# Kernel optimization log

Measured on AMD Instinct MI355X. Metric: run time of the kernel, lower is better.

## Reference

```python
import jax, jax.numpy as jnp
import numpy as np

N, E = 50000, 800000
IN_CH, N_HID, OUT_CH = 128, 256, 128
DROPOUT_P = 0.5


def gcn_conv(x, src, dst, ew, W, b, num_nodes):
    # PyG GCNConv with edge_weight: symmetric normalization with self-loops.
    loop = jnp.arange(num_nodes)
    s = jnp.concatenate([src, loop])
    d = jnp.concatenate([dst, loop])
    w = jnp.concatenate([ew, jnp.ones((num_nodes,), ew.dtype)])
    deg = jax.ops.segment_sum(w, d, num_segments=num_nodes)  # [N]
    dinv = jnp.where(deg > 0, jax.lax.rsqrt(deg), 0.0)
    norm = dinv[s] * w * dinv[d]                             # [E+N]
    h = x @ W                                                # [N, out]
    msg = h[s] * norm[:, None]                               # [E+N, out]
    out = jax.ops.segment_sum(msg, d, num_segments=num_nodes)
    return out + b


def setup_inputs() -> dict:
    key = jax.random.key(0)
    ks = jax.random.split(key, 8)
    x = jax.random.normal(ks[0], (N, IN_CH), dtype=jnp.float32)
    edge_index = jax.random.randint(ks[1], (2, E), 0, N, dtype=jnp.int64)
    weight = jax.random.uniform(ks[2], (E,), dtype=jnp.float32)
    # GCNConv params (glorot weights, zero bias)
    s1 = (6.0 / (IN_CH + N_HID)) ** 0.5
    s2 = (6.0 / (N_HID + OUT_CH)) ** 0.5
    W1 = jax.random.uniform(ks[3], (IN_CH, N_HID), jnp.float32, -s1, s1)
    b1 = jnp.zeros((N_HID,), jnp.float32)
    W2 = jax.random.uniform(ks[4], (N_HID, OUT_CH), jnp.float32, -s2, s2)
    b2 = jnp.zeros((OUT_CH,), jnp.float32)
    return {"x": x, "edge_index": edge_index, "weight": weight,
            "W1": W1, "b1": b1, "W2": W2, "b2": b2}


def reference(x, edge_index, weight, W1, b1, W2, b2):
    src, dst = edge_index[0], edge_index[1]
    h = jax.nn.relu(gcn_conv(x, src, dst, weight, W1, b1, N))
    # F.dropout(x, p) with training=True (torch default); fixed key for determinism
    keep = jax.random.bernoulli(jax.random.key(42), 1.0 - DROPOUT_P, h.shape)
    h = jnp.where(keep, h / (1.0 - DROPOUT_P), 0.0)
    return gcn_conv(h, src, dst, weight, W2, b2, N)
```

## Files before the change

### kernel.cpp

```cpp
#include <hip/hip_runtime.h>
#include <hip/hip_bf16.h>
#include <cstdint>

#define INCH 128
#define NHID 256
#define OUTCH 128

typedef unsigned short u16;
typedef unsigned long long u64;
typedef __attribute__((ext_vector_type(8))) short s8v;
typedef __attribute__((ext_vector_type(4))) float f4v;

__device__ __forceinline__ void bsplit(float a, u16& hi, u16& lo) {
    unsigned u = __float_as_uint(a);
    unsigned r = (u + 0x7fffu + ((u >> 16) & 1u)) >> 16;
    hi = (u16)r;
    float res = a - __uint_as_float(r << 16);
    unsigned u2 = __float_as_uint(res);
    lo = (u16)((u2 + 0x7fffu + ((u2 >> 16) & 1u)) >> 16);
}

__device__ __forceinline__ unsigned rotl32(unsigned x, int d) {
    return (x << d) | (x >> (32 - d));
}

__device__ __forceinline__ void threefry2x32(unsigned k0, unsigned k1,
                                             unsigned x0, unsigned x1,
                                             unsigned& o0, unsigned& o1) {
    unsigned ks2 = k0 ^ k1 ^ 0x1BD11BDAu;
#define TF_R(r) { x0 += x1; x1 = rotl32(x1, (r)); x1 ^= x0; }
    x0 += k0; x1 += k1;
    TF_R(13) TF_R(15) TF_R(26) TF_R(6)
    x0 += k1; x1 += ks2 + 1u;
    TF_R(17) TF_R(29) TF_R(16) TF_R(24)
    x0 += ks2; x1 += k0 + 2u;
    TF_R(13) TF_R(15) TF_R(26) TF_R(6)
    x0 += k0; x1 += k1 + 3u;
    TF_R(17) TF_R(29) TF_R(16) TF_R(24)
    x0 += k1; x1 += ks2 + 4u;
    TF_R(13) TF_R(15) TF_R(26) TF_R(6)
    x0 += ks2; x1 += k0 + 5u;
#undef TF_R
    o0 = x0; o1 = x1;
}

__global__ __launch_bounds__(256) void k_mask(unsigned* __restrict__ mask, int nwords) {
    int i = blockIdx.x * 256 + threadIdx.x;
    if (i >= nwords) return;
    unsigned base = (unsigned)i * 32u;
    unsigned m = 0;
#pragma unroll
    for (int b = 0; b < 32; ++b) {
        unsigned o0, o1;
        threefry2x32(0u, 42u, 0u, base + (unsigned)b, o0, o1);
        m |= ((((o0 ^ o1) >> 31) ^ 1u) & 1u) << b;
    }
    mask[i] = m;
}

__global__ void k_init(u64* packed, int N) {
    int i = blockIdx.x * blockDim.x + threadIdx.x;
    if (i < N) packed[i] = 0ull;
}

__global__ void k_hist64(const int4* __restrict__ dst4, const float4* __restrict__ w4,
                         u64* packed, int E4) {
    int i = blockIdx.x * blockDim.x + threadIdx.x;
    if (i < E4) {
        int4 d = dst4[i];
        float4 ww = w4[i];
        const u64 one = 1ull << 32;
        atomicAdd(&packed[d.x], one | (u64)__float2uint_rn(ww.x * 16777216.0f));
        atomicAdd(&packed[d.y], one | (u64)__float2uint_rn(ww.y * 16777216.0f));
        atomicAdd(&packed[d.z], one | (u64)__float2uint_rn(ww.z * 16777216.0f));
        atomicAdd(&packed[d.w], one | (u64)__float2uint_rn(ww.w * 16777216.0f));
    }
}

__global__ void k_dinv_cnt(const u64* __restrict__ packed, float* __restrict__ dinv,
                           int* __restrict__ cnt, int N) {
    int i = blockIdx.x * blockDim.x + threadIdx.x;
    if (i < N) {
        u64 p = packed[i];
        float deg = 1.0f + (float)(unsigned)(p & 0xffffffffull) * (1.0f / 16777216.0f);
        dinv[i] = rsqrtf(deg);
        cnt[i] = (int)(p >> 32);
    }
}

__global__ void scan_block(const int* __restrict__ cnt, int* __restrict__ rowptr,
                           int* __restrict__ bsum, int N) {
    __shared__ int s[256];
    int t = threadIdx.x;
    int i = blockIdx.x * 256 + t;
    int v = (i < N) ? cnt[i] : 0;
    s[t] = v;
    __syncthreads();
    for (int off = 1; off < 256; off <<= 1) {
        int tv = (t >= off) ? s[t - off] : 0;
        __syncthreads();
        s[t] += tv;
        __syncthreads();
    }
    if (i < N) rowptr[i] = s[t] - v;
    if (t == 255) bsum[blockIdx.x] = s[255];
}

__global__ void scan_partials(int* bsum, int nb) {
    __shared__ int s[256];
    int t = threadIdx.x;
    int v = (t < nb) ? bsum[t] : 0;
    s[t] = v;
    __syncthreads();
    for (int off = 1; off < 256; off <<= 1) {
        int tv = (t >= off) ? s[t - off] : 0;
        __syncthreads();
        s[t] += tv;
        __syncthreads();
    }
    if (t < nb) bsum[t] = s[t] - v;
}

__global__ void scan_add(int* rowptr, int* cursor, const int* __restrict__ bsum,
                         int N, int E) {
    int i = blockIdx.x * 256 + threadIdx.x;
    if (i < N) {
        int r = rowptr[i] + bsum[blockIdx.x];
        rowptr[i] = r;
        cursor[i] = r;
    }
    if (i == N) rowptr[N] = E;
}

__global__ void k_place(const int* __restrict__ src, const int* __restrict__ dst,
                        const float* __restrict__ w, const float* __restrict__ dinv,
                        int* cursor, int2* __restrict__ cv, int E) {
    int e = blockIdx.x * blockDim.x + threadIdx.x;
    if (e < E) {
        int s = src[e], d = dst[e];
        float nrm = dinv[s] * w[e] * dinv[d];
        int pos = atomicAdd(&cursor[d], 1);
        cv[pos] = make_int2(s, __float_as_int(nrm));
    }
}

__global__ void conv_wt(const float* __restrict__ W, u16* __restrict__ Wh,
                        u16* __restrict__ Wl, int K, int N) {
    int i = blockIdx.x * 256 + threadIdx.x;
    if (i >= K * N) return;
    int k = i / N, n = i % N;
    u16 hi, lo;
    bsplit(W[i], hi, lo);
    Wh[(size_t)n * K + k] = hi;
    Wl[(size_t)n * K + k] = lo;
}

template <int BM, int BN, bool ACT>
__global__ __launch_bounds__(256) void gemm_mfma(
    const u16* __restrict__ Ah, const u16* __restrict__ Al,
    const u16* __restrict__ Bh, const u16* __restrict__ Bl,
    const float* __restrict__ bias, const unsigned* __restrict__ mask,
    u16* __restrict__ Ch, u16* __restrict__ Cl, float* __restrict__ Cf,
    int M, int Ntot, int K) {
    constexpr int WN = BN / 2;
    constexpr int MFRAG = BM / 32;
    constexpr int NFRAG = WN / 16;
    __shared__ u16 Alh[BM][40], All[BM][40];
    __shared__ u16 Blh[BN][40], Bll[BN][40];

    const int tid = threadIdx.x;
    const int lane = tid & 63;
    const int w = tid >> 6;
    const int wm = (w >> 1) * (BM / 2);
    const int wn = (w & 1) * WN;
    const int l15 = lane & 15;
    const int kh = lane >> 4;
    const int row0 = blockIdx.y * BM;
    const int col0 = blockIdx.x * BN;

    f4v acc[MFRAG][NFRAG];
#pragma unroll
    for (int f = 0; f < MFRAG; ++f)
#pragma unroll
        for (int g = 0; g < NFRAG; ++g) acc[f][g] = (f4v){0.f, 0.f, 0.f, 0.f};

    for (int k0 = 0; k0 < K; k0 += 32) {
#pragma unroll
        for (int c = tid; c < BM * 4; c += 256) {
            int m = c >> 2, ko = (c & 3) * 8;
            int gm = row0 + m;
            uint4 vh = make_uint4(0, 0, 0, 0), vl = make_uint4(0, 0, 0, 0);
            if (gm < M) {
                size_t gi = (size_t)gm * K + k0 + ko;
                vh = *reinterpret_cast<const uint4*>(&Ah[gi]);
                vl = *reinterpret_cast<const uint4*>(&Al[gi]);
            }
            *reinterpret_cast<uint4*>(&Alh[m][ko]) = vh;
            *reinterpret_cast<uint4*>(&All[m][ko]) = vl;
        }
#pragma unroll
        for (int c = tid; c < BN * 4; c += 256) {
            int n = c >> 2, ko = (c & 3) * 8;
            size_t gi = (size_t)(col0 + n) * K + k0 + ko;
            *reinterpret_cast<uint4*>(&Blh[n][ko]) = *reinterpret_cast<const uint4*>(&Bh[gi]);
            *reinterpret_cast<uint4*>(&Bll[n][ko]) = *reinterpret_cast<const uint4*>(&Bl[gi]);
        }
        __syncthreads();

        s8v afh[MFRAG], afl[MFRAG], bfh[NFRAG], bfl[NFRAG];
#pragma unroll
        for (int f = 0; f < MFRAG; ++f) {
            afh[f] = *reinterpret_cast<const s8v*>(&Alh[wm + f * 16 + l15][kh * 8]);
            afl[f] = *reinterpret_cast<const s8v*>(&All[wm + f * 16 + l15][kh * 8]);
        }
#pragma unroll
        for (int g = 0; g < NFRAG; ++g) {
            bfh[g] = *reinterpret_cast<const s8v*>(&Blh[wn + g * 16 + l15][kh * 8]);
            bfl[g] = *reinterpret_cast<const s8v*>(&Bll[wn + g * 16 + l15][kh * 8]);
        }
#pragma unroll
        for (int f = 0; f < MFRAG; ++f)
#pragma unroll
            for (int g = 0; g < NFRAG; ++g) {
                acc[f][g] = __builtin_amdgcn_mfma_f32_16x16x32_bf16(afl[f], bfh[g], acc[f][g], 0, 0, 0);
                acc[f][g] = __builtin_amdgcn_mfma_f32_16x16x32_bf16(afh[f], bfl[g], acc[f][g], 0, 0, 0);
                acc[f][g] = __builtin_amdgcn_mfma_f32_16x16x32_bf16(afh[f], bfh[g], acc[f][g], 0, 0, 0);
            }
        __syncthreads();
    }

#pragma unroll
    for (int f = 0; f < MFRAG; ++f) {
#pragma unroll
        for (int g = 0; g < NFRAG; ++g) {
#pragma unroll
            for (int r = 0; r < 4; ++r) {
                int gr = row0 + wm + f * 16 + kh * 4 + r;
                if (gr >= M) continue;
                int gc = col0 + wn + g * 16 + l15;
                float v = acc[f][g][r];
                if (ACT) {
                    v = fmaxf(v + bias[gc], 0.f);
                    unsigned j = (unsigned)gr * (unsigned)Ntot + (unsigned)gc;
                    unsigned keep = (mask[j >> 5] >> (j & 31u)) & 1u;
                    v = keep ? v * 2.f : 0.f;
                    u16 hi, lo;
                    bsplit(v, hi, lo);
                    Ch[(size_t)gr * Ntot + gc] = hi;
                    Cl[(size_t)gr * Ntot + gc] = lo;
                } else {
                    Cf[(size_t)gr * Ntot + gc] = v;
                }
            }
        }
    }
}

template <bool SPLIT>
__global__ __launch_bounds__(256) void k_aggregate4(const float4* __restrict__ h4,
                                                    const float* __restrict__ dinv,
                                                    const int* __restrict__ rowptr,
                                                    const int2* __restrict__ cv,
                                                    const float* __restrict__ bias,
                                                    float4* __restrict__ out4,
                                                    u16* __restrict__ outh,
                                                    u16* __restrict__ outl, int N) {
    int node = blockIdx.x * 8 + (threadIdx.x >> 5);
    int lane = threadIdx.x & 31;
    if (node >= N) return;
    float di = dinv[node];
    float s = di * di;
    float4 self = h4[(size_t)node * 32 + lane];
    float4 acc;
    acc.x = self.x * s; acc.y = self.y * s; acc.z = self.z * s; acc.w = self.w * s;
    if (!SPLIT && bias) {
        float4 b = reinterpret_cast<const float4*>(bias)[lane];
        acc.x += b.x; acc.y += b.y; acc.z += b.z; acc.w += b.w;
    }
    int p0 = rowptr[node], p1 = rowptr[node + 1];
    int p = p0;
    for (; p + 8 <= p1; p += 8) {
        int2 e0 = cv[p + 0], e1 = cv[p + 1], e2 = cv[p + 2], e3 = cv[p + 3];
        int2 e4 = cv[p + 4], e5 = cv[p + 5], e6 = cv[p + 6], e7 = cv[p + 7];
        float4 g0 = h4[(size_t)e0.x * 32 + lane];
        float4 g1 = h4[(size_t)e1.x * 32 + lane];
        float4 g2 = h4[(size_t)e2.x * 32 + lane];
        float4 g3 = h4[(size_t)e3.x * 32 + lane];
        float4 g4 = h4[(size_t)e4.x * 32 + lane];
        float4 g5 = h4[(size_t)e5.x * 32 + lane];
        float4 g6 = h4[(size_t)e6.x * 32 + lane];
        float4 g7 = h4[(size_t)e7.x * 32 + lane];
#define ACC(gv, ev) { float v = __int_as_float(ev.y); \
        acc.x = fmaf(gv.x, v, acc.x); acc.y = fmaf(gv.y, v, acc.y); \
        acc.z = fmaf(gv.z, v, acc.z); acc.w = fmaf(gv.w, v, acc.w); }
        ACC(g0, e0) ACC(g1, e1) ACC(g2, e2) ACC(g3, e3)
        ACC(g4, e4) ACC(g5, e5) ACC(g6, e6) ACC(g7, e7)
    }
    for (; p < p1; ++p) {
        int2 e = cv[p];
        float4 g = h4[(size_t)e.x * 32 + lane];
        ACC(g, e)
    }
#undef ACC
    if (SPLIT) {
        ushort4 hv, lv;
        bsplit(acc.x, hv.x, lv.x);
        bsplit(acc.y, hv.y, lv.y);
        bsplit(acc.z, hv.z, lv.z);
        bsplit(acc.w, hv.w, lv.w);
        reinterpret_cast<ushort4*>(outh)[(size_t)node * 32 + lane] = hv;
        reinterpret_cast<ushort4*>(outl)[(size_t)node * 32 + lane] = lv;
    } else {
        out4[(size_t)node * 32 + lane] = acc;
    }
}

extern "C" void kernel_launch(void* const* d_in, const int* in_sizes, int n_in,
                              void* d_out, int out_size, void* d_ws, size_t ws_size,
                              hipStream_t stream) {
    (void)n_in; (void)out_size; (void)ws_size;
    const float* x  = (const float*)d_in[0];
    const int*   ei = (const int*)d_in[1];
    const float* w  = (const float*)d_in[2];
    const float* W1 = (const float*)d_in[3];
    const float* b1 = (const float*)d_in[4];
    const float* W2 = (const float*)d_in[5];
    const float* b2 = (const float*)d_in[6];
    float* out = (float*)d_out;

    int N = in_sizes[0] / INCH;
    int E = in_sizes[1] / 2;
    const int* src = ei;
    const int* dst = ei + E;

    char* ws = (char*)d_ws;
    size_t off = 0;
    auto alloc = [&](size_t bytes) -> char* {
        size_t p = (off + 255) & ~(size_t)255;
        off = p + bytes;
        return ws + p;
    };
    u64*      packed = (u64*)     alloc((size_t)N * 8);
    float*    dinv   = (float*)   alloc((size_t)N * 4);
    int*      cnt    = (int*)     alloc((size_t)N * 4);
    int*      rowptr = (int*)     alloc((size_t)(N + 1) * 4);
    int*      bsum   = (int*)     alloc(1024);
    int2*     cv     = (int2*)    alloc((size_t)E * 8);
    unsigned* mask   = (unsigned*)alloc((size_t)N * NHID / 8);
    u16*      axh    = (u16*)     alloc((size_t)N * INCH * 2);
    u16*      axl    = (u16*)     alloc((size_t)N * INCH * 2);
    u16*      hdh    = (u16*)     alloc((size_t)N * NHID * 2);
    u16*      hdl    = (u16*)     alloc((size_t)N * NHID * 2);
    u16*      w1h    = (u16*)     alloc((size_t)INCH * NHID * 2);
    u16*      w1l    = (u16*)     alloc((size_t)INCH * NHID * 2);
    u16*      w2h    = (u16*)     alloc((size_t)NHID * OUTCH * 2);
    u16*      w2l    = (u16*)     alloc((size_t)NHID * OUTCH * 2);
    float*    g2     = (float*)axh;

    int nb = (N + 255) / 256;
    int eb = (E + 255) / 256;
    int eb4 = (E / 4 + 255) / 256;
    int nwords = N * NHID / 32;

    k_init<<<nb, 256, 0, stream>>>(packed, N);
    k_hist64<<<eb4, 256, 0, stream>>>((const int4*)dst, (const float4*)w, packed, E / 4);
    k_dinv_cnt<<<nb, 256, 0, stream>>>(packed, dinv, cnt, N);
    scan_block<<<nb, 256, 0, stream>>>(cnt, rowptr, bsum, N);
    scan_partials<<<1, 256, 0, stream>>>(bsum, nb);
    scan_add<<<nb, 256, 0, stream>>>(rowptr, cnt, bsum, N, E);
    k_place<<<eb, 256, 0, stream>>>(src, dst, w, dinv, cnt, cv, E);
    conv_wt<<<(INCH * NHID + 255) / 256, 256, 0, stream>>>(W1, w1h, w1l, INCH, NHID);
    conv_wt<<<(NHID * OUTCH + 255) / 256, 256, 0, stream>>>(W2, w2h, w2l, NHID, OUTCH);
    k_mask<<<(nwords + 255) / 256, 256, 0, stream>>>(mask, nwords);

    int ab = (N + 7) / 8;

    k_aggregate4<true><<<ab, 256, 0, stream>>>((const float4*)x, dinv, rowptr, cv,
                                               nullptr, nullptr, axh, axl, N);
    dim3 gg1(NHID / 128, (N + 63) / 64);
    gemm_mfma<64, 128, true><<<gg1, 256, 0, stream>>>(axh, axl, w1h, w1l, b1, mask,
                                                      hdh, hdl, nullptr, N, NHID, INCH);

    dim3 gg2(OUTCH / 64, (N + 63) / 64);
    gemm_mfma<64, 64, false><<<gg2, 256, 0, stream>>>(hdh, hdl, w2h, w2l, nullptr, nullptr,
                                                      nullptr, nullptr, g2, N, OUTCH, NHID);
    k_aggregate4<false><<<ab, 256, 0, stream>>>((const float4*)g2, dinv, rowptr, cv,
                                                b2, (float4*)out, nullptr, nullptr, N);
}
```

Baseline: 380.7 us.

## Gather neighbor features in bf16 and restructure GEMM to 64x64 tiles with K=128

Result: slower. 394.8 us (+3.7%).

```diff
diff --git a/kernel.cpp b/kernel.cpp
--- a/kernel.cpp
+++ b/kernel.cpp
@@ -10,14 +10,18 @@
 typedef unsigned long long u64;
 typedef __attribute__((ext_vector_type(8))) short s8v;
 typedef __attribute__((ext_vector_type(4))) float f4v;
+
+__device__ __forceinline__ u16 tob(float a) {
+    unsigned u = __float_as_uint(a);
+    return (u16)((u + 0x7fffu + ((u >> 16) & 1u)) >> 16);
+}
 
 __device__ __forceinline__ void bsplit(float a, u16& hi, u16& lo) {
     unsigned u = __float_as_uint(a);
     unsigned r = (u + 0x7fffu + ((u >> 16) & 1u)) >> 16;
     hi = (u16)r;
     float res = a - __uint_as_float(r << 16);
-    unsigned u2 = __float_as_uint(res);
-    lo = (u16)((u2 + 0x7fffu + ((u2 >> 16) & 1u)) >> 16);
+    lo = tob(res);
 }
 
 __device__ __forceinline__ unsigned rotl32(unsigned x, int d) {
@@ -155,39 +159,50 @@
     Wl[(size_t)n * K + k] = lo;
 }
 
-template <int BM, int BN, bool ACT>
-__global__ __launch_bounds__(256) void gemm_mfma(
+__global__ __launch_bounds__(256) void k_tobf16(const float4* __restrict__ in,
+                                                uint4* __restrict__ outb, int n8) {
+    int i = blockIdx.x * 256 + threadIdx.x;
+    if (i >= n8) return;
+    float4 a = in[i * 2], b = in[i * 2 + 1];
+    uint4 o;
+    o.x = (unsigned)tob(a.x) | ((unsigned)tob(a.y) << 16);
+    o.y = (unsigned)tob(a.z) | ((unsigned)tob(a.w) << 16);
+    o.z = (unsigned)tob(b.x) | ((unsigned)tob(b.y) << 16);
+    o.w = (unsigned)tob(b.z) | ((unsigned)tob(b.w) << 16);
+    outb[i] = o;
+}
+
+template <int MODE>
+__global__ __launch_bounds__(256) void gemm_mfma3(
     const u16* __restrict__ Ah, const u16* __restrict__ Al,
     const u16* __restrict__ Bh, const u16* __restrict__ Bl,
     const float* __restrict__ bias, const unsigned* __restrict__ mask,
-    u16* __restrict__ Ch, u16* __restrict__ Cl, float* __restrict__ Cf,
+    const float* __restrict__ dinv,
+    u16* __restrict__ Ch, u16* __restrict__ Cl,
+    u16* __restrict__ Cb, float* __restrict__ Sp,
     int M, int Ntot, int K) {
-    constexpr int WN = BN / 2;
-    constexpr int MFRAG = BM / 32;
-    constexpr int NFRAG = WN / 16;
-    __shared__ u16 Alh[BM][40], All[BM][40];
-    __shared__ u16 Blh[BN][40], Bll[BN][40];
+    __shared__ u16 Alh[64][136], All[64][136], Blh[64][136], Bll[64][136];
 
     const int tid = threadIdx.x;
     const int lane = tid & 63;
     const int w = tid >> 6;
-    const int wm = (w >> 1) * (BM / 2);
-    const int wn = (w & 1) * WN;
+    const int wm = (w >> 1) * 32;
+    const int wn = (w & 1) * 32;
     const int l15 = lane & 15;
     const int kh = lane >> 4;
-    const int row0 = blockIdx.y * BM;
-    const int col0 = blockIdx.x * BN;
-
-    f4v acc[MFRAG][NFRAG];
-#pragma unroll
-    for (int f = 0; f < MFRAG; ++f)
-#pragma unroll
-        for (int g = 0; g < NFRAG; ++g) acc[f][g] = (f4v){0.f, 0.f, 0.f, 0.f};
-
-    for (int k0 = 0; k0 < K; k0 += 32) {
-#pragma unroll
-        for (int c = tid; c < BM * 4; c += 256) {
-            int m = c >> 2, ko = (c & 3) * 8;
+    const int row0 = blockIdx.y * 64;
+    const int col0 = blockIdx.x * 64;
+
+    f4v acc[2][2];
+#pragma unroll
+    for (int f = 0; f < 2; ++f)
+#pragma unroll
+        for (int g = 0; g < 2; ++g) acc[f][g] = (f4v){0.f, 0.f, 0.f, 0.f};
+
+    for (int k0 = 0; k0 < K; k0 += 128) {
+#pragma unroll
+        for (int q = tid; q < 1024; q += 256) {
+            int m = q >> 4, ko = (q & 15) * 8;
             int gm = row0 + m;
             uint4 vh = make_uint4(0, 0, 0, 0), vl = make_uint4(0, 0, 0, 0);
             if (gm < M) {
@@ -199,47 +214,50 @@
             *reinterpret_cast<uint4*>(&All[m][ko]) = vl;
         }
 #pragma unroll
-        for (int c = tid; c < BN * 4; c += 256) {
-            int n = c >> 2, ko = (c & 3) * 8;
+        for (int q = tid; q < 1024; q += 256) {
+            int n = q >> 4, ko = (q & 15) * 8;
             size_t gi = (size_t)(col0 + n) * K + k0 + ko;
             *reinterpret_cast<uint4*>(&Blh[n][ko]) = *reinterpret_cast<const uint4*>(&Bh[gi]);
             *reinterpret_cast<uint4*>(&Bll[n][ko]) = *reinterpret_cast<const uint4*>(&Bl[gi]);
         }
         __syncthreads();
 
-        s8v afh[MFRAG], afl[MFRAG], bfh[NFRAG], bfl[NFRAG];
-#pragma unroll
-        for (int f = 0; f < MFRAG; ++f) {
-            afh[f] = *reinterpret_cast<const s8v*>(&Alh[wm + f * 16 + l15][kh * 8]);
-            afl[f] = *reinterpret_cast<const s8v*>(&All[wm + f * 16 + l15][kh * 8]);
+#pragma unroll
+        for (int ks = 0; ks < 4; ++ks) {
+            s8v afh[2], afl[2], bfh[2], bfl[2];
+#pragma unroll
+            for (int f = 0; f < 2; ++f) {
+                afh[f] = *reinterpret_cast<const s8v*>(&Alh[wm + f * 16 + l15][kh * 8 + ks * 32]);
+                afl[f] = *reinterpret_cast<const s8v*>(&All[wm + f * 16 + l15][kh * 8 + ks * 32]);
+            }
+#pragma unroll
+            for (int g = 0; g < 2; ++g) {
+                bfh[g] = *reinterpret_cast<const s8v*>(&Blh[wn + g * 16 + l15][kh * 8 + ks * 32]);
+                bfl[g] = *reinterpret_cast<const s8v*>(&Bll[wn + g * 16 + l15][kh * 8 + ks * 32]);
+            }
+#pragma unroll
+            for (int f = 0; f < 2; ++f)
+#pragma unroll
+                for (int g = 0; g < 2; ++g) {
+                    acc[f][g] = __builtin_amdgcn_mfma_f32_16x16x32_bf16(afl[f], bfh[g], acc[f][g], 0, 0, 0);
+                    acc[f][g] = __builtin_amdgcn_mfma_f32_16x16x32_bf16(afh[f], bfl[g], acc[f][g], 0, 0, 0);
+                    acc[f][g] = __builtin_amdgcn_mfma_f32_16x16x32_bf16(afh[f], bfh[g], acc[f][g], 0, 0, 0);
+                }
         }
-#pragma unroll
-        for (int g = 0; g < NFRAG; ++g) {
-            bfh[g] = *reinterpret_cast<const s8v*>(&Blh[wn + g * 16 + l15][kh * 8]);
-            bfl[g] = *reinterpret_cast<const s8v*>(&Bll[wn + g * 16 + l15][kh * 8]);
-        }
-#pragma unroll
-        for (int f = 0; f < MFRAG; ++f)
-#pragma unroll
-            for (int g = 0; g < NFRAG; ++g) {
-                acc[f][g] = __builtin_amdgcn_mfma_f32_16x16x32_bf16(afl[f], bfh[g], acc[f][g], 0, 0, 0);
-                acc[f][g] = __builtin_amdgcn_mfma_f32_16x16x32_bf16(afh[f], bfl[g], acc[f][g], 0, 0, 0);
-                acc[f][g] = __builtin_amdgcn_mfma_f32_16x16x32_bf16(afh[f], bfh[g], acc[f][g], 0, 0, 0);
-            }
-        __syncthreads();
-    }
-
-#pragma unroll
-    for (int f = 0; f < MFRAG; ++f) {
-#pragma unroll
-        for (int g = 0; g < NFRAG; ++g) {
+        __syncthreads();
+    }
+
+#pragma unroll
+    for (int f = 0; f < 2; ++f) {
+#pragma unroll
+        for (int g = 0; g < 2; ++g) {
 #pragma unroll
             for (int r = 0; r < 4; ++r) {
                 int gr = row0 + wm + f * 16 + kh * 4 + r;
                 if (gr >= M) continue;
                 int gc = col0 + wn + g * 16 + l15;
                 float v = acc[f][g][r];
-                if (ACT) {
+                if (MODE == 0) {
                     v = fmaxf(v + bias[gc], 0.f);
                     unsigned j = (unsigned)gr * (unsigned)Ntot + (unsigned)gc;
                     unsigned keep = (mask[j >> 5] >> (j & 31u)) & 1u;
@@ -249,7 +267,9 @@
                     Ch[(size_t)gr * Ntot + gc] = hi;
                     Cl[(size_t)gr * Ntot + gc] = lo;
                 } else {
-                    Cf[(size_t)gr * Ntot + gc] = v;
+                    float d = dinv[gr];
+                    Cb[(size_t)gr * Ntot + gc] = tob(v);
+                    Sp[(size_t)gr * Ntot + gc] = fmaf(v, d * d, bias[gc]);
                 }
             }
         }
@@ -257,61 +277,81 @@
 }
 
 template <bool SPLIT>
-__global__ __launch_bounds__(256) void k_aggregate4(const float4* __restrict__ h4,
-                                                    const float* __restrict__ dinv,
-                                                    const int* __restrict__ rowptr,
-                                                    const int2* __restrict__ cv,
-                                                    const float* __restrict__ bias,
-                                                    float4* __restrict__ out4,
-                                                    u16* __restrict__ outh,
-                                                    u16* __restrict__ outl, int N) {
-    int node = blockIdx.x * 8 + (threadIdx.x >> 5);
-    int lane = threadIdx.x & 31;
+__global__ __launch_bounds__(256) void k_agg_b(const uint4* __restrict__ gb,
+                                               const float4* __restrict__ selfs,
+                                               const float* __restrict__ dinv,
+                                               const int* __restrict__ rowptr,
+                                               const int2* __restrict__ cv,
+                                               uint4* __restrict__ outh,
+                                               uint4* __restrict__ outl,
+                                               float4* __restrict__ outf, int N) {
+    int node = blockIdx.x * 16 + (threadIdx.x >> 4);
+    int l = threadIdx.x & 15;
     if (node >= N) return;
-    float di = dinv[node];
-    float s = di * di;
-    float4 self = h4[(size_t)node * 32 + lane];
-    float4 acc;
-    acc.x = self.x * s; acc.y = self.y * s; acc.z = self.z * s; acc.w = self.w * s;
-    if (!SPLIT && bias) {
-        float4 b = reinterpret_cast<const float4*>(bias)[lane];
-        acc.x += b.x; acc.y += b.y; acc.z += b.z; acc.w += b.w;
-    }
+    float4 s0 = selfs[(size_t)node * 32 + l * 2];
+    float4 s1 = selfs[(size_t)node * 32 + l * 2 + 1];
+    float a0, a1, a2, a3, a4, a5, a6, a7;
+    if (SPLIT) {
+        float d = dinv[node], sc = d * d;
+        a0 = s0.x * sc; a1 = s0.y * sc; a2 = s0.z * sc; a3 = s0.w * sc;
+        a4 = s1.x * sc; a5 = s1.y * sc; a6 = s1.z * sc; a7 = s1.w * sc;
+    } else {
+        a0 = s0.x; a1 = s0.y; a2 = s0.z; a3 = s0.w;
+        a4 = s1.x; a5 = s1.y; a6 = s1.z; a7 = s1.w;
+    }
+#define ACCB(gv, vv) { float v = (vv); \
+    a0 = fmaf(__uint_as_float((gv).x << 16), v, a0); \
+    a1 = fmaf(__uint_as_float((gv).x & 0xffff0000u), v, a1); \
+    a2 = fmaf(__uint_as_float((gv).y << 16), v, a2); \
+    a3 = fmaf(__uint_as_float((gv).y & 0xffff0000u), v, a3); \
+    a4 = fmaf(__uint_as_float((gv).z << 16), v, a4); \
+    a5 = fmaf(__uint_as_float((gv).z & 0xffff0000u), v, a5); \
+    a6 = fmaf(__uint_as_float((gv).w << 16), v, a6); \
+    a7 = fmaf(__uint_as_float((gv).w & 0xffff0000u), v, a7); }
     int p0 = rowptr[node], p1 = rowptr[node + 1];
     int p = p0;
     for (; p + 8 <= p1; p += 8) {
         int2 e0 = cv[p + 0], e1 = cv[p + 1], e2 = cv[p + 2], e3 = cv[p + 3];
         int2 e4 = cv[p + 4], e5 = cv[p + 5], e6 = cv[p + 6], e7 = cv[p + 7];
-        float4 g0 = h4[(size_t)e0.x * 32 + lane];
-        float4 g1 = h4[(size_t)e1.x * 32 + lane];
-        float4 g2 = h4[(size_t)e2.x * 32 + lane];
-        float4 g3 = h4[(size_t)e3.x * 32 + lane];
-        float4 g4 = h4[(size_t)e4.x * 32 + lane];
-        float4 g5 = h4[(size_t)e5.x * 32 + lane];
-        float4 g6 = h4[(size_t)e6.x * 32 + lane];
-        float4 g7 = h4[(size_t)e7.x * 32 + lane];
-#define ACC(gv, ev) { float v = __int_as_float(ev.y); \
-        acc.x = fmaf(gv.x, v, acc.x); acc.y = fmaf(gv.y, v, acc.y); \
-        acc.z = fmaf(gv.z, v, acc.z); acc.w = fmaf(gv.w, v, acc.w); }
-        ACC(g0, e0) ACC(g1, e1) ACC(g2, e2) ACC(g3, e3)
-        ACC(g4, e4) ACC(g5, e5) ACC(g6, e6) ACC(g7, e7)
+        uint4 g0 = gb[(size_t)e0.x * 16 + l];
+        uint4 g1 = gb[(size_t)e1.x * 16 + l];
+        uint4 g2 = gb[(size_t)e2.x * 16 + l];
+        uint4 g3 = gb[(size_t)e3.x * 16 + l];
+        uint4 g4 = gb[(size_t)e4.x * 16 + l];
+        uint4 g5 = gb[(size_t)e5.x * 16 + l];
+        uint4 g6 = gb[(size_t)e6.x * 16 + l];
+        uint4 g7 = gb[(size_t)e7.x * 16 + l];
+        ACCB(g0, __int_as_float(e0.y)) ACCB(g1, __int_as_float(e1.y))
+        ACCB(g2, __int_as_float(e2.y)) ACCB(g3, __int_as_float(e3.y))
+        ACCB(g4, __int_as_float(e4.y)) ACCB(g5, __int_as_float(e5.y))
+        ACCB(g6, __int_as_float(e6.y)) ACCB(g7, __int_as_float(e7.y))
     }
     for (; p < p1; ++p) {
         int2 e = cv[p];
-        float4 g = h4[(size_t)e.x * 32 + lane];
-        ACC(g, e)
-    }
-#undef ACC
+        uint4 g = gb[(size_t)e.x * 16 + l];
+        ACCB(g, __int_as_float(e.y))
+    }
+#undef ACCB
     if (SPLIT) {
-        ushort4 hv, lv;
-        bsplit(acc.x, hv.x, lv.x);
-        bsplit(acc.y, hv.y, lv.y);
-        bsplit(acc.z, hv.z, lv.z);
-        bsplit(acc.w, hv.w, lv.w);
-        reinterpret_cast<ushort4*>(outh)[(size_t)node * 32 + lane] = hv;
-        reinterpret_cast<ushort4*>(outl)[(size_t)node * 32 + lane] = lv;
+        u16 h[8], lo[8];
+        bsplit(a0, h[0], lo[0]); bsplit(a1, h[1], lo[1]);
+        bsplit(a2, h[2], lo[2]); bsplit(a3, h[3], lo[3]);
+        bsplit(a4, h[4], lo[4]); bsplit(a5, h[5], lo[5]);
+        bsplit(a6, h[6], lo[6]); bsplit(a7, h[7], lo[7]);
+        uint4 oh, ol;
+        oh.x = (unsigned)h[0] | ((unsigned)h[1] << 16);
+        oh.y = (unsigned)h[2] | ((unsigned)h[3] << 16);
+        oh.z = (unsigned)h[4] | ((unsigned)h[5] << 16);
+        oh.w = (unsigned)h[6] | ((unsigned)h[7] << 16);
+        ol.x = (unsigned)lo[0] | ((unsigned)lo[1] << 16);
+        ol.y = (unsigned)lo[2] | ((unsigned)lo[3] << 16);
+        ol.z = (unsigned)lo[4] | ((unsigned)lo[5] << 16);
+        ol.w = (unsigned)lo[6] | ((unsigned)lo[7] << 16);
+        outh[(size_t)node * 16 + l] = oh;
+        outl[(size_t)node * 16 + l] = ol;
     } else {
-        out4[(size_t)node * 32 + lane] = acc;
+        outf[(size_t)node * 32 + l * 2]     = make_float4(a0, a1, a2, a3);
+        outf[(size_t)node * 32 + l * 2 + 1] = make_float4(a4, a5, a6, a7);
     }
 }
 
@@ -347,6 +387,7 @@
     int*      bsum   = (int*)     alloc(1024);
     int2*     cv     = (int2*)    alloc((size_t)E * 8);
     unsigned* mask   = (unsigned*)alloc((size_t)N * NHID / 8);
+    u16*      xb     = (u16*)     alloc((size_t)N * INCH * 2);
     u16*      axh    = (u16*)     alloc((size_t)N * INCH * 2);
     u16*      axl    = (u16*)     alloc((size_t)N * INCH * 2);
     u16*      hdh    = (u16*)     alloc((size_t)N * NHID * 2);
@@ -355,7 +396,8 @@
     u16*      w1l    = (u16*)     alloc((size_t)INCH * NHID * 2);
     u16*      w2h    = (u16*)     alloc((size_t)NHID * OUTCH * 2);
     u16*      w2l    = (u16*)     alloc((size_t)NHID * OUTCH * 2);
-    float*    g2     = (float*)axh;
+    u16*      g2b    = xb;
+    float*    sp     = (float*)axh;
 
     int nb = (N + 255) / 256;
     int eb = (E + 255) / 256;
@@ -372,18 +414,21 @@
     conv_wt<<<(INCH * NHID + 255) / 256, 256, 0, stream>>>(W1, w1h, w1l, INCH, NHID);
     conv_wt<<<(NHID * OUTCH + 255) / 256, 256, 0, stream>>>(W2, w2h, w2l, NHID, OUTCH);
     k_mask<<<(nwords + 255) / 256, 256, 0, stream>>>(mask, nwords);
-
-    int ab = (N + 7) / 8;
-
-    k_aggregate4<true><<<ab, 256, 0, stream>>>((const float4*)x, dinv, rowptr, cv,
-                                               nullptr, nullptr, axh, axl, N);
-    dim3 gg1(NHID / 128, (N + 63) / 64);
-    gemm_mfma<64, 128, true><<<gg1, 256, 0, stream>>>(axh, axl, w1h, w1l, b1, mask,
-                                                      hdh, hdl, nullptr, N, NHID, INCH);
-
+    k_tobf16<<<(N * INCH / 8 + 255) / 256, 256, 0, stream>>>((const float4*)x, (uint4*)xb,
+                                                             N * INCH / 8);
+
+    int ab = (N + 15) / 16;
+
+    k_agg_b<true><<<ab, 256, 0, stream>>>((const uint4*)xb, (const float4*)x, dinv,
+                                          rowptr, cv, (uint4*)axh, (uint4*)axl,
+                                          nullptr, N);
+    dim3 gg1(NHID / 64, (N + 63) / 64);
+    gemm_mfma3<0><<<gg1, 256, 0, stream>>>(axh, axl, w1h, w1l, b1, mask, nullptr,
+                                           hdh, hdl, nullptr, nullptr, N, NHID, INCH);
     dim3 gg2(OUTCH / 64, (N + 63) / 64);
-    gemm_mfma<64, 64, false><<<gg2, 256, 0, stream>>>(hdh, hdl, w2h, w2l, nullptr, nullptr,
-                                                      nullptr, nullptr, g2, N, OUTCH, NHID);
-    k_aggregate4<false><<<ab, 256, 0, stream>>>((const float4*)g2, dinv, rowptr, cv,
-                                                b2, (float4*)out, nullptr, nullptr, N);
-}
+    gemm_mfma3<1><<<gg2, 256, 0, stream>>>(hdh, hdl, w2h, w2l, b2, nullptr, dinv,
+                                           nullptr, nullptr, g2b, sp, N, OUTCH, NHID);
+    k_agg_b<false><<<ab, 256, 0, stream>>>((const uint4*)g2b, (const float4*)sp, nullptr,
+                                           rowptr, cv, nullptr, nullptr,
+                                           (float4*)out, N);
+}
```
